# Optimization experiments

Hardware: AMD Instinct MI355X
Metric: run time of the kernel (lower is better)

Reference implementation:

```python
import jax, jax.numpy as jnp
import numpy as np
import math

B, T, D, H = 2, 2048, 1024, 16
HD = D // H


def setup_inputs() -> dict:
    key = jax.random.key(0)
    k1, k2, k3 = jax.random.split(key, 3)
    x = jax.random.normal(k1, (B, T, D), dtype=jnp.float32)
    # weights scaled like typical init to keep activations sane
    w_qkv = jax.random.normal(k2, (D, 3 * D), dtype=jnp.float32) / math.sqrt(D)
    w_out = jax.random.normal(k3, (D, D), dtype=jnp.float32) / math.sqrt(D)
    return {"x": x, "w_qkv": w_qkv, "w_out": w_out}


def reference(x, w_qkv, w_out):
    b, t, d = x.shape
    h, hd = H, HD
    qkv = x @ w_qkv                                # (b, t, 3d)
    qkv = qkv.reshape(b, t, h, 3 * hd).transpose(0, 2, 1, 3)  # (b, h, t, 3hd)
    q, k, v = jnp.split(qkv, 3, axis=-1)           # each (b, h, t, hd)
    scaled = jnp.einsum('bhqd,bhkd->bhqk', q, k) / math.sqrt(hd)
    # causal mask: strictly upper triangle -> -inf (as in torch.triu(full(-inf),1))
    causal = jnp.tril(jnp.ones((t, t), dtype=bool))
    scaled = jnp.where(causal, scaled, -jnp.inf)
    attn = jax.nn.softmax(scaled, axis=-1)
    vals = jnp.einsum('bhqk,bhkd->bhqd', attn, v)  # (b, h, t, hd)
    # NOTE: original reshapes (b,h,t,hd)->(b,t,h*hd) WITHOUT permuting heads back.
    vals = vals.reshape(b, t, h * hd)
    return vals @ w_out
```

## Files before the change

### kernel.cpp

```cpp
#include <hip/hip_runtime.h>
#include <hip/hip_bf16.h>
#include <math.h>

#define BB 2
#define TT 2048
#define DD 1024
#define HH 16
#define HDD 64

typedef __attribute__((ext_vector_type(8))) short short8;
typedef __attribute__((ext_vector_type(4))) float f32x4;
typedef __attribute__((ext_vector_type(16))) float f32x16;
typedef __attribute__((ext_vector_type(4))) unsigned u32x4;

#define PART_SPLIT 843
#define PART_BYTES 17408

__device__ __forceinline__ short f2bf(float f) {
  __hip_bfloat16 h = __float2bfloat16(f);
  return *reinterpret_cast<short*>(&h);
}

__device__ __forceinline__ float bf2f(short s) {
  unsigned u = ((unsigned)(unsigned short)s) << 16;
  return __builtin_bit_cast(float, u);
}

__device__ __forceinline__ float exp2_fast(float x) {
#if __has_builtin(__builtin_amdgcn_exp2f)
  return __builtin_amdgcn_exp2f(x);
#else
  float r;
  asm("v_exp_f32 %0, %1" : "=v"(r) : "v"(x));
  return r;
#endif
}

__device__ __forceinline__ void gload_lds16(const void* g, void* l) {
  __builtin_amdgcn_global_load_lds(
      (const __attribute__((address_space(1))) unsigned int*)g,
      (__attribute__((address_space(3))) unsigned int*)l, 16, 0, 0);
}

__global__ __launch_bounds__(256) void prep(
    const float* __restrict__ x, const float* __restrict__ w_qkv,
    const float* __restrict__ w_out, short* __restrict__ xb,
    short* __restrict__ wqkvT, short* __restrict__ woutT) {
  __shared__ float tile[32][33];
  const int bid = blockIdx.x;
  const int tid = threadIdx.x;
  if (bid < 2048) {
    int i = bid * 256 + tid;
    const float4* pp = (const float4*)x + (size_t)i * 2;
    float4 a = pp[0], bq = pp[1];
    short8 o;
    o[0] = f2bf(a.x); o[1] = f2bf(a.y); o[2] = f2bf(a.z); o[3] = f2bf(a.w);
    o[4] = f2bf(bq.x); o[5] = f2bf(bq.y); o[6] = f2bf(bq.z); o[7] = f2bf(bq.w);
    *((short8*)xb + i) = o;
    return;
  }
  const float* W;
  short* WT;
  int R, C, bx, by;
  if (bid < 2048 + 3072) {
    int t = bid - 2048;
    bx = t % 96; by = t / 96;
    W = w_qkv; WT = wqkvT; R = 1024; C = 3072;
  } else {
    int t = bid - 5120;
    bx = t & 31; by = t >> 5;
    W = w_out; WT = woutT; R = 1024; C = 1024;
  }
  const int c0 = bx * 32, r0 = by * 32;
  const int tx = tid & 31, ty = tid >> 5;
#pragma unroll
  for (int i = 0; i < 32; i += 8)
    tile[ty + i][tx] = W[(size_t)(r0 + ty + i) * C + c0 + tx];
  __syncthreads();
#pragma unroll
  for (int i = 0; i < 32; i += 8)
    WT[(size_t)(c0 + ty + i) * R + r0 + tx] = f2bf(tile[tx][ty + i]);
}

__global__ __launch_bounds__(256) void vtrans(const short* __restrict__ qkv,
                                              short* __restrict__ vtg) {
  const int t0 = blockIdx.x * 64;
  const int h = blockIdx.y, b = blockIdx.z;
  __shared__ __align__(16) short sm[64 * 64];
  const int tid = threadIdx.x;
  const short* Vg = qkv + (size_t)(b * TT) * 3072 + h * 192 + 128;
#pragma unroll
  for (int r2 = 0; r2 < 2; ++r2) {
    int c = tid + r2 * 256;
    int t = c >> 3, d0 = (c & 7) * 8;
    short8 v = *(const short8*)(Vg + (size_t)(t0 + t) * 3072 + d0);
#pragma unroll
    for (int j = 0; j < 8; ++j) {
      int d = d0 + j;
      int byte = (d << 7) + ((t * 2) ^ (((d >> 3) & 7) << 4));
      *(short*)((char*)sm + byte) = v[j];
    }
  }
  __syncthreads();
  short* outp = vtg + (size_t)(b * HH + h) * HDD * TT + t0;
#pragma unroll
  for (int r2 = 0; r2 < 2; ++r2) {
    int c = tid + r2 * 256;
    int d = c >> 3, tc = c & 7;
    int byte = (d << 7) + ((tc ^ ((d >> 3) & 7)) << 4);
    short8 v = *(const short8*)((char*)sm + byte);
    *(short8*)(outp + (size_t)d * TT + tc * 8) = v;
  }
}

template <bool OUT_BF16>
__global__ __launch_bounds__(256) void gemm_bf16_mfma(
    const short* __restrict__ A, const short* __restrict__ BT,
    void* __restrict__ Cv, int M, int N, int K) {
  constexpr int BM = 128, BN = 128, BK = 64;
  __shared__ __align__(16) short As[BM * BK];
  __shared__ __align__(16) short Bs[BN * BK];

  const int nbx = N / BN;
  const int nwg = nbx * (M / BM);
  int bid = blockIdx.x;
  {
    int q = nwg >> 3;
    bid = (bid & 7) * q + (bid >> 3);
  }
  const int m0 = (bid / nbx) * BM;
  const int n0 = (bid % nbx) * BN;

  const int tid = threadIdx.x;
  const int lane = tid & 63;
  const int l15 = lane & 15;
  const int g4 = lane >> 4;
  const int wm = tid >> 7;
  const int wn = (tid >> 6) & 1;
  const int swz = (l15 & 7) << 4;

  f32x4 acc[4][4];
#pragma unroll
  for (int i = 0; i < 4; ++i)
#pragma unroll
    for (int j = 0; j < 4; ++j) acc[i][j] = (f32x4){0.f, 0.f, 0.f, 0.f};

  for (int k0 = 0; k0 < K; k0 += BK) {
    __syncthreads();
#pragma unroll
    for (int r = 0; r < 4; ++r) {
      int c = tid + r * 256;
      int row = c >> 3, cc = c & 7;
      int sc = (cc ^ (row & 7)) * 8;
      gload_lds16(A + (size_t)(m0 + row) * K + k0 + sc, (char*)As + c * 16);
    }
#pragma unroll
    for (int r = 0; r < 4; ++r) {
      int c = tid + r * 256;
      int row = c >> 3, cc = c & 7;
      int sc = (cc ^ (row & 7)) * 8;
      gload_lds16(BT + (size_t)(n0 + row) * K + k0 + sc, (char*)Bs + c * 16);
    }
    __syncthreads();

#pragma unroll
    for (int kk = 0; kk < 2; ++kk) {
      short8 af[4], bfr[4];
#pragma unroll
      for (int i = 0; i < 4; ++i) {
        int row = wm * 64 + i * 16 + l15;
        af[i] = *(const short8*)((const char*)As + row * 128 +
                                 (((kk * 4 + g4) << 4) ^ swz));
      }
#pragma unroll
      for (int j = 0; j < 4; ++j) {
        int row = wn * 64 + j * 16 + l15;
        bfr[j] = *(const short8*)((const char*)Bs + row * 128 +
                                  (((kk * 4 + g4) << 4) ^ swz));
      }
#pragma unroll
      for (int i = 0; i < 4; ++i)
#pragma unroll
        for (int j = 0; j < 4; ++j)
          acc[i][j] = __builtin_amdgcn_mfma_f32_16x16x32_bf16(
              af[i], bfr[j], acc[i][j], 0, 0, 0);
    }
  }

#pragma unroll
  for (int i = 0; i < 4; ++i) {
#pragma unroll
    for (int j = 0; j < 4; ++j) {
#pragma unroll
      for (int r = 0; r < 4; ++r) {
        size_t idx = (size_t)(m0 + wm * 64 + i * 16 + g4 * 4 + r) * N +
                     n0 + wn * 64 + j * 16 + l15;
        if (OUT_BF16)
          ((short*)Cv)[idx] = f2bf(acc[i][j][r]);
        else
          ((float*)Cv)[idx] = acc[i][j][r];
      }
    }
  }
}

#define MAKE_PA(dst, P, B)                                                        \
  {                                                                               \
    unsigned a_, b_, c_, d_;                                                      \
    asm("v_cvt_pk_bf16_f32 %0, %1, %2" : "=v"(a_) : "v"(P[B + 0]), "v"(P[B + 1]));\
    asm("v_cvt_pk_bf16_f32 %0, %1, %2" : "=v"(b_) : "v"(P[B + 4]), "v"(P[B + 5]));\
    asm("v_permlane32_swap_b32 %0, %1" : "+v"(a_), "+v"(b_));                     \
    asm("v_cvt_pk_bf16_f32 %0, %1, %2" : "=v"(c_) : "v"(P[B + 2]), "v"(P[B + 3]));\
    asm("v_cvt_pk_bf16_f32 %0, %1, %2" : "=v"(d_) : "v"(P[B + 6]), "v"(P[B + 7]));\
    asm("v_permlane32_swap_b32 %0, %1" : "+v"(c_), "+v"(d_));                     \
    u32x4 uv_ = {a_, c_, b_, d_};                                                 \
    dst = __builtin_bit_cast(short8, uv_);                                        \
  }

__global__ __launch_bounds__(256) void attn_flash8(
    const short* __restrict__ qkv, const short* __restrict__ vtg,
    short* __restrict__ vals, char* __restrict__ partsA,
    char* __restrict__ partsB, float* __restrict__ mldiag) {
  const int bid = blockIdx.x;
  const int xcd = bid & 7;
  const int j   = bid >> 3;
  const int g   = xcd + ((j & 3) << 3);
  const int c   = 71 - (j >> 2);
  int kh = 0;
  while ((kh + 1) * (kh + 2) <= c) ++kh;
  const int u   = c - kh * (kh + 1);
  const int dlt = (u >= kh + 1) ? 1 : 0;
  const int p   = 2 * kh + dlt;
  const int ci  = u - dlt * (kh + 1);
  const int cnt = kh + 1;
  const int h = g & 15, b = g >> 4;
  const int nt  = 2 * p + 2;
  const int it0 = ci * nt / cnt;
  const int it1 = (ci + 1) * nt / cnt;

  const int tid = threadIdx.x;
  const int w = tid >> 6, lane = tid & 63;
  const int l31 = lane & 31;
  const int hi5 = lane >> 5;
  const int sw7 = lane & 7;

  __shared__ __align__(16) short Ks[2][64 * 64];
  __shared__ __align__(16) short Vs[2][64 * 64];

  const size_t bhbase = (size_t)(b * TT) * 3072 + (size_t)h * 192;

  const float SSC = 0.18033688011112042f;

  const int c2 = tid + 256;
  const int r1 = tid >> 3, s1 = tid & 7;
  const int r2 = c2 >> 3,  s2 = c2 & 7;
  const size_t kgo1 = (size_t)r1 * 3072 + ((s1 ^ (r1 & 7)) * 8);
  const size_t kgo2 = (size_t)r2 * 3072 + ((s2 ^ (r2 & 7)) * 8);
  const size_t vgo1 = (size_t)r1 * TT + ((s1 ^ (r1 & 7)) * 8);
  const size_t vgo2 = (size_t)r2 * TT + ((s2 ^ (r2 & 7)) * 8);
  char* const ldsK0 = (char*)Ks[0] + tid * 16;
  char* const ldsK1 = (char*)Ks[1] + tid * 16;
  char* const ldsV0 = (char*)Vs[0] + tid * 16;
  char* const ldsV1 = (char*)Vs[1] + tid * 16;

  const short* kptr = qkv + bhbase + 64 + (size_t)(it0 * 64) * 3072;
  const short* vptr = vtg + (size_t)(b * HH + h) * HDD * TT + it0 * 64;

  auto STAGE = [&](int buf) {
    char* kl = buf ? ldsK1 : ldsK0;
    char* vl = buf ? ldsV1 : ldsV0;
    gload_lds16(kptr + kgo1, kl);
    gload_lds16(kptr + kgo2, kl + 4096);
    gload_lds16(vptr + vgo1, vl);
    gload_lds16(vptr + vgo2, vl + 4096);
    kptr += 64 * 3072;
    vptr += 64;
  };

  short8 qf[4];
  {
    const short* Qp = qkv + bhbase +
                      (size_t)(p * 128 + w * 32 + l31) * 3072 + hi5 * 8;
#pragma unroll
    for (int ks = 0; ks < 4; ++ks) {
      short8 raw = *(const short8*)(Qp + ks * 16);
#pragma unroll
      for (int jj = 0; jj < 8; ++jj) qf[ks][jj] = f2bf(bf2f(raw[jj]) * SSC);
    }
  }

  float lsum = 0.f;
  f32x16 oacc0 = 0.f, oacc1 = 0.f;

  STAGE(0);
  int cur = 0;

#pragma unroll 1
  for (int it = it0; it < it1; ++it) {
    __syncthreads();
    if (it + 1 < it1) STAGE(cur ^ 1);

    const char* ksb = cur ? (const char*)Ks[1] : (const char*)Ks[0];
    const char* vsb = cur ? (const char*)Vs[1] : (const char*)Vs[0];

    f32x16 sA = 0.f, sB = 0.f;
    __builtin_amdgcn_s_setprio(1);
#pragma unroll
    for (int ks = 0; ks < 4; ++ks) {
      int slot = (ks * 2 + hi5);
      const char* kb0 = ksb + l31 * 128 + ((slot ^ sw7) << 4);
      short8 kf0 = *(const short8*)(kb0);
      short8 kf1 = *(const short8*)(kb0 + 32 * 128);
      sA = __builtin_amdgcn_mfma_f32_32x32x16_bf16(kf0, qf[ks], sA, 0, 0, 0);
      sB = __builtin_amdgcn_mfma_f32_32x32x16_bf16(kf1, qf[ks], sB, 0, 0, 0);
    }
    __builtin_amdgcn_s_setprio(0);

    if (it * 64 + 63 > p * 128 + w * 32) {
      const int qg = p * 128 + w * 32 + l31;
#pragma unroll
      for (int r = 0; r < 16; ++r) {
        int kr = it * 64 + (r & 3) + 8 * (r >> 2) + 4 * hi5;
        if (kr > qg) sA[r] = -INFINITY;
        if (kr + 32 > qg) sB[r] = -INFINITY;
      }
    }

    float ts0 = 0.f, ts1 = 0.f, ts2 = 0.f, ts3 = 0.f;
#pragma unroll
    for (int r = 0; r < 16; r += 2) {
      float eA0 = exp2_fast(sA[r]);
      float eA1 = exp2_fast(sA[r + 1]);
      float eB0 = exp2_fast(sB[r]);
      float eB1 = exp2_fast(sB[r + 1]);
      sA[r] = eA0; sA[r + 1] = eA1;
      sB[r] = eB0; sB[r + 1] = eB1;
      ts0 += eA0; ts1 += eA1;
      ts2 += eB0; ts3 += eB1;
    }
    lsum += (ts0 + ts1) + (ts2 + ts3);

    short8 pa0, pa1, pa2, pa3;
    MAKE_PA(pa0, sA, 0);
    MAKE_PA(pa1, sA, 8);
    MAKE_PA(pa2, sB, 0);
    MAKE_PA(pa3, sB, 8);

    __builtin_amdgcn_s_setprio(1);
#pragma unroll
    for (int dtile = 0; dtile < 2; ++dtile) {
      const char* vb = vsb + (dtile * 32 + l31) * 128;
      short8 vf0 = *(const short8*)(vb + (((0 * 2 + hi5) ^ sw7) << 4));
      short8 vf1 = *(const short8*)(vb + (((1 * 2 + hi5) ^ sw7) << 4));
      short8 vf2 = *(const short8*)(vb + (((2 * 2 + hi5) ^ sw7) << 4));
      short8 vf3 = *(const short8*)(vb + (((3 * 2 + hi5) ^ sw7) << 4));
      if (dtile == 0) {
        oacc0 = __builtin_amdgcn_mfma_f32_32x32x16_bf16(pa0, vf0, oacc0, 0, 0, 0);
        oacc0 = __builtin_amdgcn_mfma_f32_32x32x16_bf16(pa1, vf1, oacc0, 0, 0, 0);
        oacc0 = __builtin_amdgcn_mfma_f32_32x32x16_bf16(pa2, vf2, oacc0, 0, 0, 0);
        oacc0 = __builtin_amdgcn_mfma_f32_32x32x16_bf16(pa3, vf3, oacc0, 0, 0, 0);
      } else {
        oacc1 = __builtin_amdgcn_mfma_f32_32x32x16_bf16(pa0, vf0, oacc1, 0, 0, 0);
        oacc1 = __builtin_amdgcn_mfma_f32_32x32x16_bf16(pa1, vf1, oacc1, 0, 0, 0);
        oacc1 = __builtin_amdgcn_mfma_f32_32x32x16_bf16(pa2, vf2, oacc1, 0, 0, 0);
        oacc1 = __builtin_amdgcn_mfma_f32_32x32x16_bf16(pa3, vf3, oacc1, 0, 0, 0);
      }
    }
    __builtin_amdgcn_s_setprio(0);

    cur ^= 1;
  }

  lsum += __shfl_xor(lsum, 32);

  const size_t gTT = (size_t)g * TT;
  if (cnt == 1) {
    float inv = 1.f / lsum;
#pragma unroll
    for (int r = 0; r < 16; ++r) {
      int qrow = (r & 3) + 8 * (r >> 2) + 4 * hi5;
      float iq = __shfl(inv, qrow, 32);
      size_t vr = (gTT + p * 128 + w * 32 + qrow) * HDD;
      vals[vr + l31] = f2bf(oacc0[r] * iq);
      vals[vr + 32 + l31] = f2bf(oacc1[r] * iq);
    }
  } else if (ci == cnt - 1) {
#pragma unroll
    for (int r = 0; r < 16; ++r) {
      int qrow = (r & 3) + 8 * (r >> 2) + 4 * hi5;
      size_t vr = (gTT + p * 128 + w * 32 + qrow) * HDD;
      vals[vr + l31] = f2bf(oacc0[r]);
      vals[vr + 32 + l31] = f2bf(oacc1[r]);
    }
    if (lane < 32) {
      int base = (g * 16 + p) * 256;
      int qr = w * 32 + lane;
      mldiag[base + 128 + qr] = lsum;
    }
  } else {
    const int PL0 = kh * (kh - 1) + dlt * kh;
    const int e = g * 56 + PL0 + ci;
    char* pp = (e < PART_SPLIT) ? (partsA + (size_t)e * PART_BYTES)
                                : (partsB + (size_t)(e - PART_SPLIT) * PART_BYTES);
    short* po = (short*)pp;
#pragma unroll
    for (int r = 0; r < 16; ++r) {
      int qrow = (r & 3) + 8 * (r >> 2) + 4 * hi5;
      int rr = w * 32 + qrow;
      po[rr * 64 + l31] = f2bf(oacc0[r]);
      po[rr * 64 + 32 + l31] = f2bf(oacc1[r]);
    }
    if (lane < 32) {
      int qr = w * 32 + lane;
      *(float*)(pp + 16896 + qr * 4) = lsum;
    }
  }
}

__global__ __launch_bounds__(256) void attn_merge3(
    short* __restrict__ vals, const char* __restrict__ partsA,
    const char* __restrict__ partsB, const float* __restrict__ mldiag) {
  const int p = 2 + blockIdx.x;
  const int g = blockIdx.y;
  const int k = p >> 1, dlt = p & 1;
  const int np = k;
  const int PL = k * (k - 1) + dlt * k;
  const int e0 = g * 56 + PL;
  const int tid = threadIdx.x;
  const int row = tid >> 1;
  const int dh = (tid & 1) << 5;

  float lacc = mldiag[(g * 16 + p) * 256 + 128 + row];

  size_t vbase = ((size_t)g * TT + p * 128 + row) * HDD + dh;
  float o[32];
  {
    short8 v0 = *(const short8*)(vals + vbase);
    short8 v1 = *(const short8*)(vals + vbase + 8);
    short8 v2 = *(const short8*)(vals + vbase + 16);
    short8 v3 = *(const short8*)(vals + vbase + 24);
#pragma unroll
    for (int jj = 0; jj < 8; ++jj) {
      o[jj] = bf2f(v0[jj]);
      o[8 + jj] = bf2f(v1[jj]);
      o[16 + jj] = bf2f(v2[jj]);
      o[24 + jj] = bf2f(v3[jj]);
    }
  }
  for (int e = 0; e < np; ++e) {
    int ee = e0 + e;
    const char* pp = (ee < PART_SPLIT)
                         ? (partsA + (size_t)ee * PART_BYTES)
                         : (partsB + (size_t)(ee - PART_SPLIT) * PART_BYTES);
    lacc += *(const float*)(pp + 16896 + row * 4);
    const short* po = (const short*)pp + row * 64 + dh;
    short8 v0 = *(const short8*)po;
    short8 v1 = *(const short8*)(po + 8);
    short8 v2 = *(const short8*)(po + 16);
    short8 v3 = *(const short8*)(po + 24);
#pragma unroll
    for (int jj = 0; jj < 8; ++jj) {
      o[jj] += bf2f(v0[jj]);
      o[8 + jj] += bf2f(v1[jj]);
      o[16 + jj] += bf2f(v2[jj]);
      o[24 + jj] += bf2f(v3[jj]);
    }
  }
  float inv = 1.f / lacc;
  short8 w0, w1, w2, w3;
#pragma unroll
  for (int jj = 0; jj < 8; ++jj) {
    w0[jj] = f2bf(o[jj] * inv);
    w1[jj] = f2bf(o[8 + jj] * inv);
    w2[jj] = f2bf(o[16 + jj] * inv);
    w3[jj] = f2bf(o[24 + jj] * inv);
  }
  *(short8*)(vals + vbase) = w0;
  *(short8*)(vals + vbase + 8) = w1;
  *(short8*)(vals + vbase + 16) = w2;
  *(short8*)(vals + vbase + 24) = w3;
}

extern "C" void kernel_launch(void* const* d_in, const int* in_sizes, int n_in,
                              void* d_out, int out_size, void* d_ws, size_t ws_size,
                              hipStream_t stream) {
  const float* x     = (const float*)d_in[0];
  const float* w_qkv = (const float*)d_in[1];
  const float* w_out = (const float*)d_in[2];
  float* out = (float*)d_out;

  char* ws = (char*)d_ws;
  short* qkvb  = (short*)(ws);
  short* valsb = (short*)(ws + 25165824);
  short* xb    = (short*)(ws + 33554432);
  short* wqkvT = (short*)(ws + 41943040);
  short* woutT = (short*)(ws + 48234496);
  short* vtg   = (short*)(ws + 50331648);
  char*  partsA = ws + 33554432;
  char*  partsB = (char*)d_out;
  float* mldiag = (float*)(ws + 58720256);

  const int M = BB * TT;

  prep<<<6144, 256, 0, stream>>>(x, w_qkv, w_out, xb, wqkvT, woutT);

  gemm_bf16_mfma<true><<<(M / 128) * (3 * DD / 128), 256, 0, stream>>>(
      xb, wqkvT, qkvb, M, 3 * DD, DD);

  {
    dim3 g(TT / 64, HH, BB);
    vtrans<<<g, 256, 0, stream>>>(qkvb, vtg);
  }

  attn_flash8<<<2304, 256, 0, stream>>>(qkvb, vtg, valsb, partsA, partsB, mldiag);
  {
    dim3 g(14, 32);
    attn_merge3<<<g, 256, 0, stream>>>(valsb, partsA, partsB, mldiag);
  }

  gemm_bf16_mfma<false><<<(M / 128) * (DD / 128), 256, 0, stream>>>(
      valsb, woutT, out, M, DD, DD);
}
```

Measured before the change: 111.3 us.

## Triple-buffer K/V tiles in flash attention with explicit vmcnt waits

Result: no change. 112.3 us (+0.9%).

```diff
diff --git a/kernel.cpp b/kernel.cpp
--- a/kernel.cpp
+++ b/kernel.cpp
@@ -217,7 +217,7 @@
     dst = __builtin_bit_cast(short8, uv_);                                        \
   }
 
-__global__ __launch_bounds__(256) void attn_flash8(
+__global__ __launch_bounds__(256) void attn_flash9(
     const short* __restrict__ qkv, const short* __restrict__ vtg,
     short* __restrict__ vals, char* __restrict__ partsA,
     char* __restrict__ partsB, float* __restrict__ mldiag) {
@@ -244,8 +244,8 @@
   const int hi5 = lane >> 5;
   const int sw7 = lane & 7;
 
-  __shared__ __align__(16) short Ks[2][64 * 64];
-  __shared__ __align__(16) short Vs[2][64 * 64];
+  __shared__ __align__(16) short Ks[3][64 * 64];
+  __shared__ __align__(16) short Vs[3][64 * 64];
 
   const size_t bhbase = (size_t)(b * TT) * 3072 + (size_t)h * 192;
 
@@ -258,17 +258,17 @@
   const size_t kgo2 = (size_t)r2 * 3072 + ((s2 ^ (r2 & 7)) * 8);
   const size_t vgo1 = (size_t)r1 * TT + ((s1 ^ (r1 & 7)) * 8);
   const size_t vgo2 = (size_t)r2 * TT + ((s2 ^ (r2 & 7)) * 8);
-  char* const ldsK0 = (char*)Ks[0] + tid * 16;
-  char* const ldsK1 = (char*)Ks[1] + tid * 16;
-  char* const ldsV0 = (char*)Vs[0] + tid * 16;
-  char* const ldsV1 = (char*)Vs[1] + tid * 16;
+  char* const ldsK[3] = {(char*)Ks[0] + tid * 16, (char*)Ks[1] + tid * 16,
+                         (char*)Ks[2] + tid * 16};
+  char* const ldsV[3] = {(char*)Vs[0] + tid * 16, (char*)Vs[1] + tid * 16,
+                         (char*)Vs[2] + tid * 16};
 
   const short* kptr = qkv + bhbase + 64 + (size_t)(it0 * 64) * 3072;
   const short* vptr = vtg + (size_t)(b * HH + h) * HDD * TT + it0 * 64;
 
   auto STAGE = [&](int buf) {
-    char* kl = buf ? ldsK1 : ldsK0;
-    char* vl = buf ? ldsV1 : ldsV0;
+    char* kl = (buf == 0) ? ldsK[0] : (buf == 1) ? ldsK[1] : ldsK[2];
+    char* vl = (buf == 0) ? ldsV[0] : (buf == 1) ? ldsV[1] : ldsV[2];
     gload_lds16(kptr + kgo1, kl);
     gload_lds16(kptr + kgo2, kl + 4096);
     gload_lds16(vptr + vgo1, vl);
@@ -293,15 +293,27 @@
   f32x16 oacc0 = 0.f, oacc1 = 0.f;
 
   STAGE(0);
+  if (it0 + 1 < it1) STAGE(1);
   int cur = 0;
 
 #pragma unroll 1
   for (int it = it0; it < it1; ++it) {
-    __syncthreads();
-    if (it + 1 < it1) STAGE(cur ^ 1);
-
-    const char* ksb = cur ? (const char*)Ks[1] : (const char*)Ks[0];
-    const char* vsb = cur ? (const char*)Vs[1] : (const char*)Vs[0];
+    if (it == it1 - 1)
+      asm volatile("s_waitcnt vmcnt(0)" ::: "memory");
+    else
+      asm volatile("s_waitcnt vmcnt(4)" ::: "memory");
+    __builtin_amdgcn_s_barrier();
+    asm volatile("" ::: "memory");
+    if (it + 2 < it1) {
+      int nb = cur + 2;
+      if (nb >= 3) nb -= 3;
+      STAGE(nb);
+    }
+
+    const char* ksb = (cur == 0) ? (const char*)Ks[0]
+                     : (cur == 1) ? (const char*)Ks[1] : (const char*)Ks[2];
+    const char* vsb = (cur == 0) ? (const char*)Vs[0]
+                     : (cur == 1) ? (const char*)Vs[1] : (const char*)Vs[2];
 
     f32x16 sA = 0.f, sB = 0.f;
     __builtin_amdgcn_s_setprio(1);
@@ -368,7 +380,7 @@
     }
     __builtin_amdgcn_s_setprio(0);
 
-    cur ^= 1;
+    cur = (cur == 2) ? 0 : cur + 1;
   }
 
   lsum += __shfl_xor(lsum, 32);
@@ -512,7 +524,7 @@
     vtrans<<<g, 256, 0, stream>>>(qkvb, vtg);
   }
 
-  attn_flash8<<<2304, 256, 0, stream>>>(qkvb, vtg, valsb, partsA, partsB, mldiag);
+  attn_flash9<<<2304, 256, 0, stream>>>(qkvb, vtg, valsb, partsA, partsB, mldiag);
   {
     dim3 g(14, 32);
     attn_merge3<<<g, 256, 0, stream>>>(valsb, partsA, partsB, mldiag);
```
